# Optimization experiments

Measured on AMD Instinct MI355X. Metric: run time of the kernel, lower is better.

Reference implementation:

```python
import jax, jax.numpy as jnp
import numpy as np

D_MODEL = 512
NHEAD = 8
HEAD_DIM = D_MODEL // NHEAD
LN_EPS = 1e-5


def setup_inputs() -> dict:
    key = jax.random.key(0)
    ks = jax.random.split(key, 6)
    S, B, D = 2048, 64, D_MODEL
    src = jax.random.normal(ks[0], (S, B, D), dtype=jnp.float32)
    seq_lengths = jax.random.randint(ks[1], (B,), 1, S + 1, dtype=jnp.int32)
    sc = 1.0 / np.sqrt(D)
    in_proj_weight = jax.random.normal(ks[2], (3 * D, D), dtype=jnp.float32) * sc
    in_proj_bias = jnp.zeros((3 * D,), dtype=jnp.float32)
    out_proj_weight = jax.random.normal(ks[3], (D, D), dtype=jnp.float32) * sc
    out_proj_bias = jnp.zeros((D,), dtype=jnp.float32)
    ln_weight = jnp.ones((D,), dtype=jnp.float32)
    ln_bias = jnp.zeros((D,), dtype=jnp.float32)
    return {
        'src': src, 'seq_lengths': seq_lengths,
        'in_proj_weight': in_proj_weight, 'in_proj_bias': in_proj_bias,
        'out_proj_weight': out_proj_weight, 'out_proj_bias': out_proj_bias,
        'ln_weight': ln_weight, 'ln_bias': ln_bias,
    }


def reference(src, seq_lengths, in_proj_weight, in_proj_bias,
              out_proj_weight, out_proj_bias, ln_weight, ln_bias):
    S, B, D = src.shape
    H, hd = NHEAD, HEAD_DIM
    # gather last valid token per batch element -> queries [B, D]
    q_in = src[seq_lengths - 1, jnp.arange(B)]
    Wq, Wk, Wv = in_proj_weight[:D], in_proj_weight[D:2 * D], in_proj_weight[2 * D:]
    bq, bk, bv = in_proj_bias[:D], in_proj_bias[D:2 * D], in_proj_bias[2 * D:]
    scale = 1.0 / jnp.sqrt(jnp.asarray(hd, src.dtype))
    q = (q_in @ Wq.T + bq).reshape(B, H, hd) * scale          # [B,H,hd]
    k = (src @ Wk.T + bk).reshape(S, B, H, hd)                # [S,B,H,hd]
    v = (src @ Wv.T + bv).reshape(S, B, H, hd)
    scores = jnp.einsum('bhd,sbhd->bhs', q, k)                # [B,H,S]
    attn = jax.nn.softmax(scores, axis=-1)
    ctx = jnp.einsum('bhs,sbhd->bhd', attn, v).reshape(B, D)  # [B,D]
    attn_out = ctx @ out_proj_weight.T + out_proj_bias        # [B,D]
    # residual: attn_out broadcasts across the sequence dim (src2 is [1,B,D])
    x = src + attn_out[None, :, :]
    mu = jnp.mean(x, axis=-1, keepdims=True)
    var = jnp.mean(jnp.square(x - mu), axis=-1, keepdims=True)
    return (x - mu) / jnp.sqrt(var + LN_EPS) * ln_weight + ln_bias
```

## Files before the change

### kernel.cpp

```cpp
#include <hip/hip_runtime.h>

#define S_LEN 2048
#define BATCH 64
#define DMODEL 512
#define NHEAD 8
#define HDIM 64
#define LN_EPS_F 1e-5f
#define QSCALE 0.125f

__global__ void __launch_bounds__(256) k_q_qk(
    const float* __restrict__ src, const int* __restrict__ seqlen,
    const float* __restrict__ w_in, const float* __restrict__ b_in,
    float* __restrict__ qk)
{
    __shared__ float xl[DMODEL];
    __shared__ float ql[256];
    const int b = blockIdx.x;
    const int y = blockIdx.y;
    const int t = threadIdx.x;
    const int last = seqlen[b] - 1;
    const float* xrow = src + ((size_t)last * BATCH + b) * DMODEL;
    for (int i = t; i < DMODEL; i += 256) xl[i] = xrow[i];
    __syncthreads();
    {
        const int d = y * 256 + t;
        const float* wr = w_in + (size_t)d * DMODEL;
        float acc = b_in[d];
        for (int i = 0; i < DMODEL; i += 4) {
            const float4 r = *reinterpret_cast<const float4*>(wr + i);
            acc += r.x * xl[i] + r.y * xl[i + 1] + r.z * xl[i + 2] + r.w * xl[i + 3];
        }
        ql[t] = acc * QSCALE;
    }
    __syncthreads();
#pragma unroll
    for (int r = 0; r < 8; r++) {
        const int hl = r >> 1;
        const int dp = (r & 1) * 256 + t;
        const int h = y * 4 + hl;
        float acc = 0.f;
#pragma unroll 16
        for (int j = 0; j < HDIM; j++)
            acc += w_in[((size_t)(DMODEL + h * HDIM + j)) * DMODEL + dp] * ql[hl * HDIM + j];
        qk[((size_t)b * NHEAD + h) * DMODEL + dp] = acc;
    }
}

__global__ void __launch_bounds__(256) k_scores(
    const float* __restrict__ src, const float* __restrict__ qk,
    float* __restrict__ scores)
{
    const int b = blockIdx.x;
    const int sb = blockIdx.y;
    const int t = threadIdx.x;
    const int wave = t >> 6, lane = t & 63;

    float qr[NHEAD][8];
    const float* qb = qk + (size_t)b * NHEAD * DMODEL + lane * 8;
#pragma unroll
    for (int h = 0; h < NHEAD; h++) {
        const float4 a = *reinterpret_cast<const float4*>(qb + h * DMODEL);
        const float4 c = *reinterpret_cast<const float4*>(qb + h * DMODEL + 4);
        qr[h][0] = a.x; qr[h][1] = a.y; qr[h][2] = a.z; qr[h][3] = a.w;
        qr[h][4] = c.x; qr[h][5] = c.y; qr[h][6] = c.z; qr[h][7] = c.w;
    }
    const int sbase = sb * 32 + wave * 8;
    float acc[64];
#pragma unroll
    for (int j = 0; j < 64; j++) acc[j] = 0.f;
#pragma unroll
    for (int i = 0; i < 8; i++) {
        const float* xrow = src + ((size_t)(sbase + i) * BATCH + b) * DMODEL + lane * 8;
        const float4 xa = *reinterpret_cast<const float4*>(xrow);
        const float4 xc = *reinterpret_cast<const float4*>(xrow + 4);
        float xf[8];
        xf[0] = xa.x; xf[1] = xa.y; xf[2] = xa.z; xf[3] = xa.w;
        xf[4] = xc.x; xf[5] = xc.y; xf[6] = xc.z; xf[7] = xc.w;
#pragma unroll
        for (int h = 0; h < NHEAD; h++) {
            float a = acc[h * 8 + i];
#pragma unroll
            for (int j = 0; j < 8; j++) a += qr[h][j] * xf[j];
            acc[h * 8 + i] = a;
        }
    }
#pragma unroll
    for (int st = 0; st < 6; st++) {
        const int m = 32 >> st;
        const int nh = 32 >> st;
        const bool hi = (lane & m) != 0;
#pragma unroll
        for (int j = 0; j < nh; j++) {
            const float keep = hi ? acc[j + nh] : acc[j];
            const float give = hi ? acc[j] : acc[j + nh];
            acc[j] = keep + __shfl_xor(give, m, 64);
        }
    }
    scores[((size_t)b * NHEAD + (lane >> 3)) * S_LEN + sbase + (lane & 7)] = acc[0];
}

__global__ void __launch_bounds__(256) k_softmax(float* __restrict__ scores)
{
    const int bh = blockIdx.x;
    const int t = threadIdx.x;
    const int wave = t >> 6, lane = t & 63;
    float* p = scores + (size_t)bh * S_LEN;
    float v[8];
    float m = -1e30f;
#pragma unroll
    for (int k = 0; k < 8; k++) { v[k] = p[t + k * 256]; m = fmaxf(m, v[k]); }
#pragma unroll
    for (int mk = 32; mk; mk >>= 1) m = fmaxf(m, __shfl_xor(m, mk, 64));
    __shared__ float redm[4], reds[4];
    if (lane == 0) redm[wave] = m;
    __syncthreads();
    m = fmaxf(fmaxf(redm[0], redm[1]), fmaxf(redm[2], redm[3]));
    float s = 0.f;
#pragma unroll
    for (int k = 0; k < 8; k++) { v[k] = __expf(v[k] - m); s += v[k]; }
#pragma unroll
    for (int mk = 32; mk; mk >>= 1) s += __shfl_xor(s, mk, 64);
    if (lane == 0) reds[wave] = s;
    __syncthreads();
    const float inv = 1.0f / (reds[0] + reds[1] + reds[2] + reds[3]);
#pragma unroll
    for (int k = 0; k < 8; k++) p[t + k * 256] = v[k] * inv;
}

__global__ void __launch_bounds__(256) k_xbar(
    const float* __restrict__ src, const float* __restrict__ attn,
    float* __restrict__ xpart)
{
    __shared__ float al[256][8];
    const int b = blockIdx.x;
    const int c = blockIdx.y;
    const int t = threadIdx.x;
    const int s0 = c * 256;
    {
        float v[8];
#pragma unroll
        for (int h = 0; h < NHEAD; h++)
            v[h] = attn[((size_t)b * NHEAD + h) * S_LEN + s0 + t];
        *reinterpret_cast<float4*>(&al[t][0]) = make_float4(v[0], v[1], v[2], v[3]);
        *reinterpret_cast<float4*>(&al[t][4]) = make_float4(v[4], v[5], v[6], v[7]);
    }
    __syncthreads();
    float acc0[NHEAD] = {0.f, 0.f, 0.f, 0.f, 0.f, 0.f, 0.f, 0.f};
    float acc1[NHEAD] = {0.f, 0.f, 0.f, 0.f, 0.f, 0.f, 0.f, 0.f};
    const float* base = src + (size_t)s0 * BATCH * DMODEL + (size_t)b * DMODEL + 2 * t;
#pragma unroll 4
    for (int i = 0; i < 256; i++) {
        const float2 xv = *reinterpret_cast<const float2*>(base + (size_t)i * BATCH * DMODEL);
        const float4 a0 = *reinterpret_cast<const float4*>(&al[i][0]);
        const float4 a1 = *reinterpret_cast<const float4*>(&al[i][4]);
        acc0[0] += a0.x * xv.x; acc1[0] += a0.x * xv.y;
        acc0[1] += a0.y * xv.x; acc1[1] += a0.y * xv.y;
        acc0[2] += a0.z * xv.x; acc1[2] += a0.z * xv.y;
        acc0[3] += a0.w * xv.x; acc1[3] += a0.w * xv.y;
        acc0[4] += a1.x * xv.x; acc1[4] += a1.x * xv.y;
        acc0[5] += a1.y * xv.x; acc1[5] += a1.y * xv.y;
        acc0[6] += a1.z * xv.x; acc1[6] += a1.z * xv.y;
        acc0[7] += a1.w * xv.x; acc1[7] += a1.w * xv.y;
    }
#pragma unroll
    for (int h = 0; h < NHEAD; h++) {
        const size_t idx = (((size_t)c * BATCH + b) * NHEAD + h) * DMODEL + 2 * t;
        *reinterpret_cast<float2*>(xpart + idx) = make_float2(acc0[h], acc1[h]);
    }
}

__global__ void __launch_bounds__(256) k_ctx(
    const float* __restrict__ xpart, const float* __restrict__ w_in,
    const float* __restrict__ b_in, float* __restrict__ ctx)
{
    __shared__ float xb[4 * DMODEL];
    const int b = blockIdx.x;
    const int y = blockIdx.y;
    const int t = threadIdx.x;
    for (int i = t; i < 4 * DMODEL; i += 256) {
        float a = 0.f;
#pragma unroll
        for (int c = 0; c < 8; c++)
            a += xpart[((size_t)c * BATCH + b) * (NHEAD * DMODEL) + y * 4 * DMODEL + i];
        xb[i] = a;
    }
    __syncthreads();
    const int e = y * 256 + t;
    const int hl = t >> 6;
    const float* wr = w_in + ((size_t)(2 * DMODEL + e)) * DMODEL;
    const float* xr = &xb[hl * DMODEL];
    float acc = b_in[2 * DMODEL + e];
    for (int d = 0; d < DMODEL; d += 4) {
        const float4 r = *reinterpret_cast<const float4*>(wr + d);
        acc += r.x * xr[d] + r.y * xr[d + 1] + r.z * xr[d + 2] + r.w * xr[d + 3];
    }
    ctx[(size_t)b * DMODEL + e] = acc;
}

__global__ void __launch_bounds__(256) k_outproj(
    const float* __restrict__ ctx, const float* __restrict__ w_out,
    const float* __restrict__ b_out, float* __restrict__ attn_out)
{
    __shared__ float cl[DMODEL];
    const int b = blockIdx.x;
    const int y = blockIdx.y;
    const int t = threadIdx.x;
    for (int i = t; i < DMODEL; i += 256) cl[i] = ctx[(size_t)b * DMODEL + i];
    __syncthreads();
    const int o = y * 256 + t;
    const float* wr = w_out + (size_t)o * DMODEL;
    float acc = b_out[o];
    for (int e = 0; e < DMODEL; e += 4) {
        const float4 r = *reinterpret_cast<const float4*>(wr + e);
        acc += r.x * cl[e] + r.y * cl[e + 1] + r.z * cl[e + 2] + r.w * cl[e + 3];
    }
    attn_out[(size_t)b * DMODEL + o] = acc;
}

__global__ void __launch_bounds__(256) k_ln(
    const float* __restrict__ src, const float* __restrict__ attn_out,
    const float* __restrict__ g, const float* __restrict__ beta,
    float* __restrict__ out)
{
    const int t = threadIdx.x;
    const int wave = t >> 6, lane = t & 63;
    const int row = blockIdx.x * 4 + wave;
    const int b = row & (BATCH - 1);
    const int d0 = lane * 8;
    const float* xp = src + (size_t)row * DMODEL + d0;
    const float4 xa = *reinterpret_cast<const float4*>(xp);
    const float4 xc = *reinterpret_cast<const float4*>(xp + 4);
    const float* ap = attn_out + (size_t)b * DMODEL + d0;
    const float4 aa = *reinterpret_cast<const float4*>(ap);
    const float4 ac = *reinterpret_cast<const float4*>(ap + 4);
    float x[8];
    x[0] = xa.x + aa.x; x[1] = xa.y + aa.y; x[2] = xa.z + aa.z; x[3] = xa.w + aa.w;
    x[4] = xc.x + ac.x; x[5] = xc.y + ac.y; x[6] = xc.z + ac.z; x[7] = xc.w + ac.w;
    float s1 = 0.f, s2 = 0.f;
#pragma unroll
    for (int j = 0; j < 8; j++) { s1 += x[j]; s2 += x[j] * x[j]; }
#pragma unroll
    for (int m = 32; m; m >>= 1) {
        s1 += __shfl_xor(s1, m, 64);
        s2 += __shfl_xor(s2, m, 64);
    }
    const float mu = s1 * (1.0f / DMODEL);
    const float var = s2 * (1.0f / DMODEL) - mu * mu;
    const float inv = rsqrtf(var + LN_EPS_F);
    const float4 ga = *reinterpret_cast<const float4*>(g + d0);
    const float4 gc = *reinterpret_cast<const float4*>(g + d0 + 4);
    const float4 ba = *reinterpret_cast<const float4*>(beta + d0);
    const float4 bc = *reinterpret_cast<const float4*>(beta + d0 + 4);
    float4 y0, y1;
    y0.x = (x[0] - mu) * inv * ga.x + ba.x;
    y0.y = (x[1] - mu) * inv * ga.y + ba.y;
    y0.z = (x[2] - mu) * inv * ga.z + ba.z;
    y0.w = (x[3] - mu) * inv * ga.w + ba.w;
    y1.x = (x[4] - mu) * inv * gc.x + bc.x;
    y1.y = (x[5] - mu) * inv * gc.y + bc.y;
    y1.z = (x[6] - mu) * inv * gc.z + bc.z;
    y1.w = (x[7] - mu) * inv * gc.w + bc.w;
    float* op = out + (size_t)row * DMODEL + d0;
    *reinterpret_cast<float4*>(op) = y0;
    *reinterpret_cast<float4*>(op + 4) = y1;
}

extern "C" void kernel_launch(void* const* d_in, const int* in_sizes, int n_in,
                              void* d_out, int out_size, void* d_ws, size_t ws_size,
                              hipStream_t stream)
{
    const float* src   = (const float*)d_in[0];
    const int*   slen  = (const int*)d_in[1];
    const float* w_in  = (const float*)d_in[2];
    const float* b_in  = (const float*)d_in[3];
    const float* w_out = (const float*)d_in[4];
    const float* b_out = (const float*)d_in[5];
    const float* g     = (const float*)d_in[6];
    const float* beta  = (const float*)d_in[7];
    float* out = (float*)d_out;

    char* ws = (char*)d_ws;
    float* qk       = (float*)(ws);
    float* scores   = (float*)(ws + (1u << 20));
    float* xpart    = (float*)(ws + 5u * (1u << 20));
    float* attn_out = (float*)(ws + 13u * (1u << 20));
    float* ctxbuf   = (float*)(ws + 13u * (1u << 20) + (1u << 17));

    k_q_qk<<<dim3(BATCH, 2), 256, 0, stream>>>(src, slen, w_in, b_in, qk);
    k_scores<<<dim3(BATCH, S_LEN / 32), 256, 0, stream>>>(src, qk, scores);
    k_softmax<<<BATCH * NHEAD, 256, 0, stream>>>(scores);
    k_xbar<<<dim3(BATCH, 8), 256, 0, stream>>>(src, scores, xpart);
    k_ctx<<<dim3(BATCH, 2), 256, 0, stream>>>(xpart, w_in, b_in, ctxbuf);
    k_outproj<<<dim3(BATCH, 2), 256, 0, stream>>>(ctxbuf, w_out, b_out, attn_out);
    k_ln<<<S_LEN * BATCH / 4, 256, 0, stream>>>(src, attn_out, g, beta, out);
}
```

Before: 661.2 us.

## Fuse scores, softmax and weighted sum into one online-softmax attention kernel

Replaces the separate score, softmax and attention-weighted-sum kernels with one flash-style kernel. Each wave streams its 64 sequence rows once, keeps a running max and sum per head, and rescales its accumulators as it goes. It writes partial weighted sums plus (max, sum) pairs for 32 chunks, which k_ctx then combines with rescaling coefficients. This removes one full pass over src and the round trip of the score matrix through memory. The cost is more exp and shuffle work per row, heavier register use, and 32 partials to reduce instead of 8.

```diff
diff --git a/kernel.cpp b/kernel.cpp
--- a/kernel.cpp
+++ b/kernel.cpp
@@ -7,6 +7,8 @@
 #define HDIM 64
 #define LN_EPS_F 1e-5f
 #define QSCALE 0.125f
+#define NCHUNK 8
+#define NCW 32
 
 __global__ void __launch_bounds__(256) k_q_qk(
     const float* __restrict__ src, const int* __restrict__ seqlen,
@@ -46,12 +48,13 @@
     }
 }
 
-__global__ void __launch_bounds__(256) k_scores(
+__global__ void __launch_bounds__(256, 2) k_attn(
     const float* __restrict__ src, const float* __restrict__ qk,
-    float* __restrict__ scores)
-{
+    float* __restrict__ xpart, float* __restrict__ ml)
+{
+    __shared__ float wt[4][32];
     const int b = blockIdx.x;
-    const int sb = blockIdx.y;
+    const int c = blockIdx.y;
     const int t = threadIdx.x;
     const int wave = t >> 6, lane = t & 63;
 
@@ -60,128 +63,145 @@
 #pragma unroll
     for (int h = 0; h < NHEAD; h++) {
         const float4 a = *reinterpret_cast<const float4*>(qb + h * DMODEL);
-        const float4 c = *reinterpret_cast<const float4*>(qb + h * DMODEL + 4);
+        const float4 d = *reinterpret_cast<const float4*>(qb + h * DMODEL + 4);
         qr[h][0] = a.x; qr[h][1] = a.y; qr[h][2] = a.z; qr[h][3] = a.w;
-        qr[h][4] = c.x; qr[h][5] = c.y; qr[h][6] = c.z; qr[h][7] = c.w;
-    }
-    const int sbase = sb * 32 + wave * 8;
-    float acc[64];
-#pragma unroll
-    for (int j = 0; j < 64; j++) acc[j] = 0.f;
-#pragma unroll
-    for (int i = 0; i < 8; i++) {
-        const float* xrow = src + ((size_t)(sbase + i) * BATCH + b) * DMODEL + lane * 8;
-        const float4 xa = *reinterpret_cast<const float4*>(xrow);
-        const float4 xc = *reinterpret_cast<const float4*>(xrow + 4);
-        float xf[8];
-        xf[0] = xa.x; xf[1] = xa.y; xf[2] = xa.z; xf[3] = xa.w;
-        xf[4] = xc.x; xf[5] = xc.y; xf[6] = xc.z; xf[7] = xc.w;
+        qr[h][4] = d.x; qr[h][5] = d.y; qr[h][6] = d.z; qr[h][7] = d.w;
+    }
+    float acc[NHEAD][8];
+#pragma unroll
+    for (int h = 0; h < NHEAD; h++)
+#pragma unroll
+        for (int k = 0; k < 8; k++) acc[h][k] = 0.f;
+    float m[NHEAD];
+#pragma unroll
+    for (int h = 0; h < NHEAD; h++) m[h] = -1e30f;
+    float m_own = -1e30f;
+    float lw = 0.f;
+    const int i_own = (lane >> 1) & 3;
+    const int sw = c * 256 + wave * 64;
+
+    for (int g = 0; g < 16; g++) {
+        float xf[4][8];
+#pragma unroll
+        for (int i = 0; i < 4; i++) {
+            const float* xr = src + ((size_t)(sw + g * 4 + i) * BATCH + b) * DMODEL + lane * 8;
+            const float4 xa = *reinterpret_cast<const float4*>(xr);
+            const float4 xc = *reinterpret_cast<const float4*>(xr + 4);
+            xf[i][0] = xa.x; xf[i][1] = xa.y; xf[i][2] = xa.z; xf[i][3] = xa.w;
+            xf[i][4] = xc.x; xf[i][5] = xc.y; xf[i][6] = xc.z; xf[i][7] = xc.w;
+        }
+        float sc[32];
+#pragma unroll
+        for (int j = 0; j < 32; j++) {
+            const int h = j >> 2, i = j & 3;
+            float a = 0.f;
+#pragma unroll
+            for (int k = 0; k < 8; k++) a += qr[h][k] * xf[i][k];
+            sc[j] = a;
+        }
+#pragma unroll
+        for (int st = 0; st < 5; st++) {
+            const int mk = 32 >> st;
+            const int nh = 16 >> st;
+            const bool hi = (lane & mk) != 0;
+#pragma unroll
+            for (int j = 0; j < nh; j++) {
+                const float keep = hi ? sc[j + nh] : sc[j];
+                const float give = hi ? sc[j] : sc[j + nh];
+                sc[j] = keep + __shfl_xor(give, mk, 64);
+            }
+        }
+        const float sfull = sc[0] + __shfl_xor(sc[0], 1, 64);
+        float tm = sfull;
+        tm = fmaxf(tm, __shfl_xor(tm, 2, 64));
+        tm = fmaxf(tm, __shfl_xor(tm, 4, 64));
+        const float m_own_new = fmaxf(m_own, tm);
+        const float fown = __expf(m_own - m_own_new);
+        const float w_own = __expf(sfull - m_own_new);
+        m_own = m_own_new;
+        lw = lw * fown + w_own;
+        wt[wave][i_own * 8 + (lane >> 3)] = w_own;
 #pragma unroll
         for (int h = 0; h < NHEAD; h++) {
-            float a = acc[h * 8 + i];
-#pragma unroll
-            for (int j = 0; j < 8; j++) a += qr[h][j] * xf[j];
-            acc[h * 8 + i] = a;
-        }
-    }
-#pragma unroll
-    for (int st = 0; st < 6; st++) {
-        const int m = 32 >> st;
-        const int nh = 32 >> st;
-        const bool hi = (lane & m) != 0;
-#pragma unroll
-        for (int j = 0; j < nh; j++) {
-            const float keep = hi ? acc[j + nh] : acc[j];
-            const float give = hi ? acc[j] : acc[j + nh];
-            acc[j] = keep + __shfl_xor(give, m, 64);
-        }
-    }
-    scores[((size_t)b * NHEAD + (lane >> 3)) * S_LEN + sbase + (lane & 7)] = acc[0];
-}
-
-__global__ void __launch_bounds__(256) k_softmax(float* __restrict__ scores)
-{
-    const int bh = blockIdx.x;
-    const int t = threadIdx.x;
-    const int wave = t >> 6, lane = t & 63;
-    float* p = scores + (size_t)bh * S_LEN;
-    float v[8];
-    float m = -1e30f;
-#pragma unroll
-    for (int k = 0; k < 8; k++) { v[k] = p[t + k * 256]; m = fmaxf(m, v[k]); }
-#pragma unroll
-    for (int mk = 32; mk; mk >>= 1) m = fmaxf(m, __shfl_xor(m, mk, 64));
-    __shared__ float redm[4], reds[4];
-    if (lane == 0) redm[wave] = m;
-    __syncthreads();
-    m = fmaxf(fmaxf(redm[0], redm[1]), fmaxf(redm[2], redm[3]));
-    float s = 0.f;
-#pragma unroll
-    for (int k = 0; k < 8; k++) { v[k] = __expf(v[k] - m); s += v[k]; }
-#pragma unroll
-    for (int mk = 32; mk; mk >>= 1) s += __shfl_xor(s, mk, 64);
-    if (lane == 0) reds[wave] = s;
-    __syncthreads();
-    const float inv = 1.0f / (reds[0] + reds[1] + reds[2] + reds[3]);
-#pragma unroll
-    for (int k = 0; k < 8; k++) p[t + k * 256] = v[k] * inv;
-}
-
-__global__ void __launch_bounds__(256) k_xbar(
-    const float* __restrict__ src, const float* __restrict__ attn,
-    float* __restrict__ xpart)
-{
-    __shared__ float al[256][8];
-    const int b = blockIdx.x;
-    const int c = blockIdx.y;
-    const int t = threadIdx.x;
-    const int s0 = c * 256;
-    {
-        float v[8];
-#pragma unroll
-        for (int h = 0; h < NHEAD; h++)
-            v[h] = attn[((size_t)b * NHEAD + h) * S_LEN + s0 + t];
-        *reinterpret_cast<float4*>(&al[t][0]) = make_float4(v[0], v[1], v[2], v[3]);
-        *reinterpret_cast<float4*>(&al[t][4]) = make_float4(v[4], v[5], v[6], v[7]);
-    }
-    __syncthreads();
-    float acc0[NHEAD] = {0.f, 0.f, 0.f, 0.f, 0.f, 0.f, 0.f, 0.f};
-    float acc1[NHEAD] = {0.f, 0.f, 0.f, 0.f, 0.f, 0.f, 0.f, 0.f};
-    const float* base = src + (size_t)s0 * BATCH * DMODEL + (size_t)b * DMODEL + 2 * t;
-#pragma unroll 4
-    for (int i = 0; i < 256; i++) {
-        const float2 xv = *reinterpret_cast<const float2*>(base + (size_t)i * BATCH * DMODEL);
-        const float4 a0 = *reinterpret_cast<const float4*>(&al[i][0]);
-        const float4 a1 = *reinterpret_cast<const float4*>(&al[i][4]);
-        acc0[0] += a0.x * xv.x; acc1[0] += a0.x * xv.y;
-        acc0[1] += a0.y * xv.x; acc1[1] += a0.y * xv.y;
-        acc0[2] += a0.z * xv.x; acc1[2] += a0.z * xv.y;
-        acc0[3] += a0.w * xv.x; acc1[3] += a0.w * xv.y;
-        acc0[4] += a1.x * xv.x; acc1[4] += a1.x * xv.y;
-        acc0[5] += a1.y * xv.x; acc1[5] += a1.y * xv.y;
-        acc0[6] += a1.z * xv.x; acc1[6] += a1.z * xv.y;
-        acc0[7] += a1.w * xv.x; acc1[7] += a1.w * xv.y;
-    }
+            const float tmh = __shfl(tm, h * 8, 64);
+            const float mn = fmaxf(m[h], tmh);
+            const float fh = __expf(m[h] - mn);
+            m[h] = mn;
+#pragma unroll
+            for (int k = 0; k < 8; k++) acc[h][k] *= fh;
+        }
+#pragma unroll
+        for (int i = 0; i < 4; i++) {
+            const float4 wa = *reinterpret_cast<const float4*>(&wt[wave][i * 8]);
+            const float4 wb = *reinterpret_cast<const float4*>(&wt[wave][i * 8 + 4]);
+            const float wv[8] = {wa.x, wa.y, wa.z, wa.w, wb.x, wb.y, wb.z, wb.w};
+#pragma unroll
+            for (int h = 0; h < NHEAD; h++)
+#pragma unroll
+                for (int k = 0; k < 8; k++) acc[h][k] += wv[h] * xf[i][k];
+        }
+    }
+    lw += __shfl_xor(lw, 2, 64);
+    lw += __shfl_xor(lw, 4, 64);
+    const int cw = c * 4 + wave;
 #pragma unroll
     for (int h = 0; h < NHEAD; h++) {
-        const size_t idx = (((size_t)c * BATCH + b) * NHEAD + h) * DMODEL + 2 * t;
-        *reinterpret_cast<float2*>(xpart + idx) = make_float2(acc0[h], acc1[h]);
+        float* xp = xpart + (((size_t)cw * BATCH + b) * NHEAD + h) * DMODEL + lane * 8;
+        *reinterpret_cast<float4*>(xp) = make_float4(acc[h][0], acc[h][1], acc[h][2], acc[h][3]);
+        *reinterpret_cast<float4*>(xp + 4) = make_float4(acc[h][4], acc[h][5], acc[h][6], acc[h][7]);
+    }
+    if ((lane & 7) == 0) {
+        const int h = lane >> 3;
+        *reinterpret_cast<float2*>(ml + (((size_t)cw * BATCH + b) * NHEAD + h) * 2) =
+            make_float2(m_own, lw);
     }
 }
 
 __global__ void __launch_bounds__(256) k_ctx(
-    const float* __restrict__ xpart, const float* __restrict__ w_in,
-    const float* __restrict__ b_in, float* __restrict__ ctx)
+    const float* __restrict__ xpart, const float* __restrict__ ml,
+    const float* __restrict__ w_in, const float* __restrict__ b_in,
+    float* __restrict__ ctx)
 {
     __shared__ float xb[4 * DMODEL];
+    __shared__ float Mh[4], Dn[4];
+    __shared__ float coef[4][NCW];
     const int b = blockIdx.x;
     const int y = blockIdx.y;
     const int t = threadIdx.x;
+    if (t < 4) {
+        const int h = y * 4 + t;
+        float M = -1e30f;
+#pragma unroll
+        for (int cw = 0; cw < NCW; cw++) {
+            const float2 v = *reinterpret_cast<const float2*>(
+                ml + (((size_t)cw * BATCH + b) * NHEAD + h) * 2);
+            M = fmaxf(M, v.x);
+        }
+        float den = 0.f;
+#pragma unroll
+        for (int cw = 0; cw < NCW; cw++) {
+            const float2 v = *reinterpret_cast<const float2*>(
+                ml + (((size_t)cw * BATCH + b) * NHEAD + h) * 2);
+            den += __expf(v.x - M) * v.y;
+        }
+        Mh[t] = M; Dn[t] = den;
+    }
+    __syncthreads();
+    if (t < 4 * NCW) {
+        const int h4 = t >> 5, cw = t & (NCW - 1);
+        const float2 v = *reinterpret_cast<const float2*>(
+            ml + (((size_t)cw * BATCH + b) * NHEAD + y * 4 + h4) * 2);
+        coef[h4][cw] = __expf(v.x - Mh[h4]) / Dn[h4];
+    }
+    __syncthreads();
     for (int i = t; i < 4 * DMODEL; i += 256) {
+        const int hl = i >> 9;
+        const int d = i & (DMODEL - 1);
         float a = 0.f;
 #pragma unroll
-        for (int c = 0; c < 8; c++)
-            a += xpart[((size_t)c * BATCH + b) * (NHEAD * DMODEL) + y * 4 * DMODEL + i];
+        for (int cw = 0; cw < NCW; cw++)
+            a += coef[hl][cw] *
+                 xpart[(((size_t)cw * BATCH + b) * NHEAD + y * 4 + hl) * DMODEL + d];
         xb[i] = a;
     }
     __syncthreads();
@@ -240,9 +260,9 @@
 #pragma unroll
     for (int j = 0; j < 8; j++) { s1 += x[j]; s2 += x[j] * x[j]; }
 #pragma unroll
-    for (int m = 32; m; m >>= 1) {
-        s1 += __shfl_xor(s1, m, 64);
-        s2 += __shfl_xor(s2, m, 64);
+    for (int mk = 32; mk; mk >>= 1) {
+        s1 += __shfl_xor(s1, mk, 64);
+        s2 += __shfl_xor(s2, mk, 64);
     }
     const float mu = s1 * (1.0f / DMODEL);
     const float var = s2 * (1.0f / DMODEL) - mu * mu;
@@ -281,16 +301,14 @@
 
     char* ws = (char*)d_ws;
     float* qk       = (float*)(ws);
-    float* scores   = (float*)(ws + (1u << 20));
-    float* xpart    = (float*)(ws + 5u * (1u << 20));
-    float* attn_out = (float*)(ws + 13u * (1u << 20));
-    float* ctxbuf   = (float*)(ws + 13u * (1u << 20) + (1u << 17));
+    float* xpart    = (float*)(ws + (1u << 20));
+    float* ml       = (float*)(ws + 33u * (1u << 20));
+    float* ctxbuf   = (float*)(ws + 34u * (1u << 20));
+    float* attn_out = (float*)(ws + 35u * (1u << 20));
 
     k_q_qk<<<dim3(BATCH, 2), 256, 0, stream>>>(src, slen, w_in, b_in, qk);
-    k_scores<<<dim3(BATCH, S_LEN / 32), 256, 0, stream>>>(src, qk, scores);
-    k_softmax<<<BATCH * NHEAD, 256, 0, stream>>>(scores);
-    k_xbar<<<dim3(BATCH, 8), 256, 0, stream>>>(src, scores, xpart);
-    k_ctx<<<dim3(BATCH, 2), 256, 0, stream>>>(xpart, w_in, b_in, ctxbuf);
+    k_attn<<<dim3(BATCH, NCHUNK), 256, 0, stream>>>(src, qk, xpart, ml);
+    k_ctx<<<dim3(BATCH, 2), 256, 0, stream>>>(xpart, ml, w_in, b_in, ctxbuf);
     k_outproj<<<dim3(BATCH, 2), 256, 0, stream>>>(ctxbuf, w_out, b_out, attn_out);
     k_ln<<<S_LEN * BATCH / 4, 256, 0, stream>>>(src, attn_out, g, beta, out);
 }
```

After: 955.1 us. 1.44x slower.
